# Performance work log

Measured on AMD Instinct MI355X. Metric: run time of the kernel, lower is better.

Reference implementation:

```python
import jax, jax.numpy as jnp
import numpy as np

NX, NY, NZ = 432, 496, 1   # grid_size (nx, ny, nz), nz must be 1
NBEV = 128                 # NUM_BEV_FEATURES
K = 4                      # NUM_K
SHRINK = 0.0025            # SHRINK_TH
BN_EPS = 1e-3


def setup_inputs():
    key = jax.random.key(0)
    ks = jax.random.split(key, 8)
    B, P, NPT, D, M = 2, 6000, 4096, 64, 1024
    pillar_features = jax.random.normal(ks[0], (B, P, D), jnp.float32)
    point_features = jax.random.normal(ks[1], (B, NPT, D), jnp.float32)
    # unique flat BEV cells per scene -> coords columns (z, y, x) as in OpenPCDet coords[:,1:4]
    coords = []
    for b in range(B):
        flat = jax.random.permutation(jax.random.fold_in(ks[2], b), NX * NY)[:P]
        y = flat // NX
        x = flat % NX
        z = jnp.zeros_like(flat)
        coords.append(jnp.stack([z, y, x], axis=1))
    voxel_coords = jnp.stack(coords, 0).astype(jnp.int32)
    adapt_w = jax.random.normal(ks[3], (NBEV // 2, D * K), jnp.float32) * 0.05  # Linear(no bias)
    mem_w = jax.random.normal(ks[4], (M, D), jnp.float32) * 0.05               # MemoryUnit slots
    bn_gamma = jnp.ones((NBEV // 2,), jnp.float32)
    bn_beta = jnp.zeros((NBEV // 2,), jnp.float32)
    return dict(pillar_features=pillar_features, point_features=point_features,
                voxel_coords=voxel_coords, adapt_w=adapt_w, mem_w=mem_w,
                bn_gamma=bn_gamma, bn_beta=bn_beta)


def _forward(pillar_features, point_features, voxel_coords, adapt_w, mem_w, bn_gamma, bn_beta):
    def per_batch(pillars, points, coords):
        # pillars [P,D], points [Np,D], coords [P,3] = (z, y, x)
        # get_score: softmax over points dim, top-k points per pillar
        score = jax.nn.softmax(pillars @ points.T, axis=1)            # [P,Np]
        _, idx = jax.lax.top_k(score, K)                              # [P,K] (indices detached)
        pts = points[idx]                                             # [P,K,D]
        # MemoryUnit (MemAE-style): softmax attention over memory, hard-shrink-relu, L1 renorm
        x = pts.reshape(-1, points.shape[1])                          # [P*K,D]
        att = jax.nn.softmax(x @ mem_w.T, axis=1)                     # [P*K,M]
        shr = jax.nn.relu(att - SHRINK) * att / (jnp.abs(att - SHRINK) + 1e-12)
        att = shr / (jnp.sum(jnp.abs(shr), axis=1, keepdims=True) + 1e-12)
        mem_out = (att @ mem_w).reshape(pillars.shape[0], -1)         # [P, K*D]
        # adapt_layer (Linear, no bias) -> BatchNorm1d (training stats over pillars) -> ReLU
        h = mem_out @ adapt_w.T                                       # [P, NBEV//2]
        mu = jnp.mean(h, axis=0)
        var = jnp.var(h, axis=0)
        h = (h - mu) / jnp.sqrt(var + BN_EPS) * bn_gamma + bn_beta
        h = jax.nn.relu(h)
        feats = jnp.concatenate([pillars, h], axis=1)                 # [P, NBEV]
        # scatter into dense BEV grid: index = z + y*nx + x (nz==1 so z==0)
        flat = coords[:, 0] + coords[:, 1] * NX + coords[:, 2]
        spatial = jnp.zeros((NBEV, NZ * NX * NY), feats.dtype).at[:, flat].set(feats.T)
        pind = jnp.zeros((3, NZ * NX * NY), feats.dtype)
        pind = pind.at[0, flat].set(coords[:, 1].astype(feats.dtype))
        pind = pind.at[1, flat].set(coords[:, 2].astype(feats.dtype))
        pind = pind.at[2, flat].set(coords[:, 0].astype(feats.dtype))
        return spatial, pind

    spatial, pind = jax.vmap(per_batch)(pillar_features, point_features, voxel_coords)
    B = spatial.shape[0]
    return spatial.reshape(B, NBEV * NZ, NY, NX), pind.reshape(B, 3 * NZ, NY, NX)


def reference(pillar_features, point_features, voxel_coords, adapt_w, mem_w, bn_gamma, bn_beta):
    return _forward(pillar_features, point_features, voxel_coords, adapt_w, mem_w, bn_gamma, bn_beta)
```

## Files before the change

kernel.cpp:

```cpp
#include <hip/hip_runtime.h>

#define NXg 432
#define NYg 496
#define SCELLS (NXg*NYg)
#define PB 6000
#define NPTS 4096
#define DD 64
#define MM 1024
#define KK 4
#define BB 2
#define NROWS (PB*KK)
#define NSEG 16
#define SEGPTS (NPTS/NSEG)
#define CHROWS 64
#define NCHNK (SEGPTS/CHROWS)
#define SHRINK_TH 0.0025f
#define BN_EPS 1e-3f
#define NEG_INF -3.402823466e38f

#define INS4(v, id, v0,v1,v2,v3, i0,i1,i2,i3) { \
    bool g0 = (v) > v0, g1 = (v) > v1, g2 = (v) > v2; \
    v3 = g2 ? v2 : (v);              i3 = g2 ? i2 : (id); \
    v2 = g2 ? (g1 ? v1 : (v)) : v2;  i2 = g2 ? (g1 ? i1 : (id)) : i2; \
    v1 = g1 ? (g0 ? v0 : (v)) : v1;  i1 = g1 ? (g0 ? i0 : (id)) : i1; \
    v0 = g0 ? (v) : v0;              i0 = g0 ? (id) : i0; \
}

__global__ __launch_bounds__(256) void k_init_inv(int* __restrict__ inv) {
    int i = blockIdx.x*256 + threadIdx.x;
    inv[i] = -1;
}

__global__ __launch_bounds__(256) void k_scatter_inv(const int* __restrict__ coords,
                                                     int* __restrict__ inv) {
    int i = blockIdx.x*256 + threadIdx.x;
    if (i >= BB*PB) return;
    int b = i / PB, p = i % PB;
    const int* c = coords + (size_t)i*3;
    int flat = c[0] + c[1]*NXg + c[2];
    inv[b*SCELLS + flat] = p;
}

__global__ __launch_bounds__(256) void k_score_topk(const float* __restrict__ pillars,
                                                    const float* __restrict__ points,
                                                    float* __restrict__ pV,
                                                    int* __restrict__ pI) {
    __shared__ float4 sPt[CHROWS*16];
    const int b = blockIdx.y;
    const int seg = blockIdx.z;
    const int t = threadIdx.x;
    const int pillar = blockIdx.x*256 + t;
    const int prow = pillar < PB ? pillar : PB-1;
    const int j0 = seg * SEGPTS;

    const float4* pil4  = (const float4*)pillars;
    const float4* ptsB4 = (const float4*)(points + (size_t)b*NPTS*DD);

    float4 wreg[16];
    #pragma unroll
    for (int d4 = 0; d4 < 16; d4++)
        wreg[d4] = pil4[((size_t)b*PB + prow)*16 + d4];

    float tv0=NEG_INF, tv1=NEG_INF, tv2=NEG_INF, tv3=NEG_INF;
    int   ti0=0, ti1=0, ti2=0, ti3=0;

    for (int ch = 0; ch < NCHNK; ch++) {
        const float4* src = ptsB4 + (size_t)(j0 + ch*CHROWS)*16;
        for (int i = t; i < CHROWS*16; i += 256)
            sPt[i] = src[i];
        __syncthreads();

        const int jb = j0 + ch*CHROWS;
        for (int j = 0; j < CHROWS; j += 2) {
            float a0 = 0.f, a1 = 0.f;
            #pragma unroll
            for (int d4 = 0; d4 < 16; d4++) {
                float4 x0 = sPt[j*16 + d4];
                float4 x1 = sPt[(j+1)*16 + d4];
                a0 += wreg[d4].x*x0.x + wreg[d4].y*x0.y + wreg[d4].z*x0.z + wreg[d4].w*x0.w;
                a1 += wreg[d4].x*x1.x + wreg[d4].y*x1.y + wreg[d4].z*x1.z + wreg[d4].w*x1.w;
            }
            if (a0 > tv3) INS4(a0, jb+j,   tv0,tv1,tv2,tv3, ti0,ti1,ti2,ti3)
            if (a1 > tv3) INS4(a1, jb+j+1, tv0,tv1,tv2,tv3, ti0,ti1,ti2,ti3)
        }
        __syncthreads();
    }

    if (pillar < PB) {
        size_t ob = (((size_t)b*NSEG + seg)*PB + pillar)*KK;
        pV[ob+0]=tv0; pV[ob+1]=tv1; pV[ob+2]=tv2; pV[ob+3]=tv3;
        pI[ob+0]=ti0; pI[ob+1]=ti1; pI[ob+2]=ti2; pI[ob+3]=ti3;
    }
}

__global__ __launch_bounds__(256) void k_merge(const float* __restrict__ pV,
                                               const int* __restrict__ pI,
                                               int* __restrict__ idxOut) {
    int i = blockIdx.x*256 + threadIdx.x;
    if (i >= BB*PB) return;
    int b = i / PB, p = i % PB;
    float fv0=NEG_INF, fv1=NEG_INF, fv2=NEG_INF, fv3=NEG_INF;
    int fi0=0, fi1=0, fi2=0, fi3=0;
    for (int s = 0; s < NSEG; s++) {
        size_t base = (((size_t)b*NSEG + s)*PB + p)*KK;
        #pragma unroll
        for (int q = 0; q < 4; q++) {
            float v = pV[base+q];
            if (v > fv3) INS4(v, pI[base+q], fv0,fv1,fv2,fv3, fi0,fi1,fi2,fi3)
        }
    }
    idxOut[(size_t)i*KK+0]=fi0; idxOut[(size_t)i*KK+1]=fi1;
    idxOut[(size_t)i*KK+2]=fi2; idxOut[(size_t)i*KK+3]=fi3;
}

__global__ __launch_bounds__(256) void k_logits(const float* __restrict__ points,
                                                const int* __restrict__ idxIn,
                                                const float* __restrict__ memw,
                                                float* __restrict__ logits,
                                                int b) {
    __shared__ float4 sX4[64*16];
    __shared__ int sId[64];
    const int t = threadIdx.x;
    const int lane = t & 63, wv = t >> 6;
    const int row0 = blockIdx.x * 64;
    const int cg = blockIdx.y * 256 + wv * 64;

    if (t < 64) sId[t] = idxIn[(size_t)b*NROWS + row0 + t];

    const float4* mw4 = (const float4*)memw;
    float4 wreg[16];
    #pragma unroll
    for (int d4 = 0; d4 < 16; d4++) wreg[d4] = mw4[(size_t)(cg + lane)*16 + d4];

    __syncthreads();
    const float4* ptsB4 = (const float4*)(points + (size_t)b*NPTS*DD);
    for (int i = t; i < 1024; i += 256) {
        int r = i >> 4, c = i & 15;
        sX4[i] = ptsB4[(size_t)sId[r]*16 + c];
    }
    __syncthreads();

    for (int r = 0; r < 64; r += 2) {
        float a0 = 0.f, a1 = 0.f;
        #pragma unroll
        for (int d4 = 0; d4 < 16; d4++) {
            float4 x0 = sX4[r*16 + d4];
            float4 x1 = sX4[(r+1)*16 + d4];
            a0 += wreg[d4].x*x0.x + wreg[d4].y*x0.y + wreg[d4].z*x0.z + wreg[d4].w*x0.w;
            a1 += wreg[d4].x*x1.x + wreg[d4].y*x1.y + wreg[d4].z*x1.z + wreg[d4].w*x1.w;
        }
        logits[(size_t)(row0 + r)*MM + cg + lane] = a0;
        logits[(size_t)(row0 + r + 1)*MM + cg + lane] = a1;
    }
}

__global__ __launch_bounds__(256) void k_mo(const float* __restrict__ logits,
                                            const float* __restrict__ memw,
                                            const float* __restrict__ adaptw,
                                            float* __restrict__ hOut,
                                            int b) {
    __shared__ __align__(16) char smem[77824];
    float4* sAtt4 = (float4*)smem;
    float4* sW4   = (float4*)(smem + 12288);
    float*  sWf   = (float*)sW4;
    __shared__ float sM[48], sRinv[48], sRsc[48];
    const int t = threadIdx.x;
    const int lane = t & 63, wv = t >> 6;
    const int p0 = blockIdx.x * 12;
    const int row0 = p0 * 4;

    const float4* lg4 = (const float4*)logits;
    #pragma unroll
    for (int rr = 0; rr < 12; rr++) {
        int r = wv*12 + rr;
        size_t base = (size_t)(row0 + r)*256;
        float4 l0 = lg4[base + lane];
        float4 l1 = lg4[base + 64 + lane];
        float4 l2 = lg4[base + 128 + lane];
        float4 l3 = lg4[base + 192 + lane];
        float m = fmaxf(fmaxf(fmaxf(l0.x,l0.y),fmaxf(l0.z,l0.w)),
                 fmaxf(fmaxf(fmaxf(l1.x,l1.y),fmaxf(l1.z,l1.w)),
                 fmaxf(fmaxf(fmaxf(l2.x,l2.y),fmaxf(l2.z,l2.w)),
                       fmaxf(fmaxf(l3.x,l3.y),fmaxf(l3.z,l3.w)))));
        #pragma unroll
        for (int off = 1; off < 64; off <<= 1) m = fmaxf(m, __shfl_xor(m, off));
        l0.x=__expf(l0.x-m); l0.y=__expf(l0.y-m); l0.z=__expf(l0.z-m); l0.w=__expf(l0.w-m);
        l1.x=__expf(l1.x-m); l1.y=__expf(l1.y-m); l1.z=__expf(l1.z-m); l1.w=__expf(l1.w-m);
        l2.x=__expf(l2.x-m); l2.y=__expf(l2.y-m); l2.z=__expf(l2.z-m); l2.w=__expf(l2.w-m);
        l3.x=__expf(l3.x-m); l3.y=__expf(l3.y-m); l3.z=__expf(l3.z-m); l3.w=__expf(l3.w-m);
        float s = (l0.x+l0.y+l0.z+l0.w) + (l1.x+l1.y+l1.z+l1.w)
                + (l2.x+l2.y+l2.z+l2.w) + (l3.x+l3.y+l3.z+l3.w);
        #pragma unroll
        for (int off = 1; off < 64; off <<= 1) s += __shfl_xor(s, off);
        float rinv = 1.f / s;
        float sh = 0.f;
        {
            float e, tt;
            e=l0.x*rinv; tt=e-SHRINK_TH; sh += tt>0.f ? e*tt/(tt+1e-12f) : 0.f;
            e=l0.y*rinv; tt=e-SHRINK_TH; sh += tt>0.f ? e*tt/(tt+1e-12f) : 0.f;
            e=l0.z*rinv; tt=e-SHRINK_TH; sh += tt>0.f ? e*tt/(tt+1e-12f) : 0.f;
            e=l0.w*rinv; tt=e-SHRINK_TH; sh += tt>0.f ? e*tt/(tt+1e-12f) : 0.f;
            e=l1.x*rinv; tt=e-SHRINK_TH; sh += tt>0.f ? e*tt/(tt+1e-12f) : 0.f;
            e=l1.y*rinv; tt=e-SHRINK_TH; sh += tt>0.f ? e*tt/(tt+1e-12f) : 0.f;
            e=l1.z*rinv; tt=e-SHRINK_TH; sh += tt>0.f ? e*tt/(tt+1e-12f) : 0.f;
            e=l1.w*rinv; tt=e-SHRINK_TH; sh += tt>0.f ? e*tt/(tt+1e-12f) : 0.f;
            e=l2.x*rinv; tt=e-SHRINK_TH; sh += tt>0.f ? e*tt/(tt+1e-12f) : 0.f;
            e=l2.y*rinv; tt=e-SHRINK_TH; sh += tt>0.f ? e*tt/(tt+1e-12f) : 0.f;
            e=l2.z*rinv; tt=e-SHRINK_TH; sh += tt>0.f ? e*tt/(tt+1e-12f) : 0.f;
            e=l2.w*rinv; tt=e-SHRINK_TH; sh += tt>0.f ? e*tt/(tt+1e-12f) : 0.f;
            e=l3.x*rinv; tt=e-SHRINK_TH; sh += tt>0.f ? e*tt/(tt+1e-12f) : 0.f;
            e=l3.y*rinv; tt=e-SHRINK_TH; sh += tt>0.f ? e*tt/(tt+1e-12f) : 0.f;
            e=l3.z*rinv; tt=e-SHRINK_TH; sh += tt>0.f ? e*tt/(tt+1e-12f) : 0.f;
            e=l3.w*rinv; tt=e-SHRINK_TH; sh += tt>0.f ? e*tt/(tt+1e-12f) : 0.f;
        }
        #pragma unroll
        for (int off = 1; off < 64; off <<= 1) sh += __shfl_xor(sh, off);
        if (lane == 0) { sM[r] = m; sRinv[r] = rinv; sRsc[r] = 1.f/(sh + 1e-12f); }
    }
    __syncthreads();

    float acc[12];
    #pragma unroll
    for (int s=0;s<12;s++) acc[s]=0.f;
    const float4* mw4 = (const float4*)memw;

    for (int tile = 0; tile < 16; tile++) {
        __syncthreads();
        for (int i = t; i < 768; i += 256) {
            int rr = i >> 4, m4 = i & 15;
            float4 lg = lg4[(size_t)(row0 + rr)*256 + tile*16 + m4];
            float m = sM[rr], rinv = sRinv[rr], rsc = sRsc[rr];
            float4 o;
            float e, tt;
            e=__expf(lg.x-m)*rinv; tt=e-SHRINK_TH; o.x = (tt>0.f ? e*tt/(tt+1e-12f) : 0.f)*rsc;
            e=__expf(lg.y-m)*rinv; tt=e-SHRINK_TH; o.y = (tt>0.f ? e*tt/(tt+1e-12f) : 0.f)*rsc;
            e=__expf(lg.z-m)*rinv; tt=e-SHRINK_TH; o.z = (tt>0.f ? e*tt/(tt+1e-12f) : 0.f)*rsc;
            e=__expf(lg.w-m)*rinv; tt=e-SHRINK_TH; o.w = (tt>0.f ? e*tt/(tt+1e-12f) : 0.f)*rsc;
            sAtt4[rr*16 + m4] = o;
        }
        #pragma unroll 4
        for (int i = t; i < 1024; i += 256) {
            int m = i >> 4, c4 = i & 15;
            sW4[m*16 + c4] = mw4[(size_t)(tile*64 + m)*16 + c4];
        }
        __syncthreads();
        #pragma unroll 4
        for (int m4 = 0; m4 < 16; m4++) {
            float w0 = sWf[(m4*4+0)*64 + lane];
            float w1 = sWf[(m4*4+1)*64 + lane];
            float w2 = sWf[(m4*4+2)*64 + lane];
            float w3 = sWf[(m4*4+3)*64 + lane];
            #pragma unroll
            for (int s = 0; s < 12; s++) {
                float4 a4 = sAtt4[(wv + 4*s)*16 + m4];
                acc[s] += a4.x*w0 + a4.y*w1 + a4.z*w2 + a4.w*w3;
            }
        }
    }
    __syncthreads();
    float* sMo = (float*)smem;
    float4* sA4 = (float4*)(smem + 12288);
    #pragma unroll
    for (int s = 0; s < 12; s++) {
        int r = wv + 4*s;
        sMo[r*64 + lane] = acc[s];
    }
    const float4* adG4 = (const float4*)adaptw;
    for (int i = t; i < 4096; i += 256) {
        int c = i >> 6, j4 = i & 63;
        sA4[c*64 + (j4 ^ (c & 15))] = adG4[c*64 + j4];
    }
    __syncthreads();
    const float4* sMo4 = (const float4*)sMo;
    float h0=0.f, h1=0.f, h2=0.f;
    #pragma unroll 8
    for (int j4 = 0; j4 < 64; j4++) {
        float4 a4 = sA4[lane*64 + (j4 ^ (lane & 15))];
        int sub = (j4 >> 4)*16 + (j4 & 15);
        float4 q0 = sMo4[(4*(wv+0))*16 + sub];
        float4 q1 = sMo4[(4*(wv+4))*16 + sub];
        float4 q2 = sMo4[(4*(wv+8))*16 + sub];
        h0 += q0.x*a4.x + q0.y*a4.y + q0.z*a4.z + q0.w*a4.w;
        h1 += q1.x*a4.x + q1.y*a4.y + q1.z*a4.z + q1.w*a4.w;
        h2 += q2.x*a4.x + q2.y*a4.y + q2.z*a4.z + q2.w*a4.w;
    }
    hOut[((size_t)b*PB + p0 + wv + 0)*DD + lane] = h0;
    hOut[((size_t)b*PB + p0 + wv + 4)*DD + lane] = h1;
    hOut[((size_t)b*PB + p0 + wv + 8)*DD + lane] = h2;
}

__global__ __launch_bounds__(256) void k_bn1(const float* __restrict__ h,
                                             float* __restrict__ pSum,
                                             float* __restrict__ pSq) {
    const int bid = blockIdx.x;
    const int b = bid >> 5, ch = bid & 31;
    const int r0 = ch*188;
    int r1 = r0 + 188; if (r1 > PB) r1 = PB;
    __shared__ float sS[4*64], sS2[4*64];
    const int t = threadIdx.x;
    const int c = t & 63, stripe = t >> 6;
    float s = 0.f, s2 = 0.f;
    for (int r = r0 + stripe; r < r1; r += 4) {
        float v = h[((size_t)b*PB + r)*DD + c];
        s += v; s2 += v*v;
    }
    sS[stripe*64 + c] = s; sS2[stripe*64 + c] = s2;
    __syncthreads();
    if (t < 64) {
        float ts = sS[t] + sS[64+t] + sS[128+t] + sS[192+t];
        float ts2 = sS2[t] + sS2[64+t] + sS2[128+t] + sS2[192+t];
        pSum[(size_t)bid*64 + t] = ts;
        pSq[(size_t)bid*64 + t] = ts2;
    }
}

__global__ __launch_bounds__(64) void k_bn2(const float* __restrict__ pSum,
                                            const float* __restrict__ pSq,
                                            const float* __restrict__ gamma,
                                            float* __restrict__ bnMu,
                                            float* __restrict__ bnScale) {
    const int b = blockIdx.x;
    const int t = threadIdx.x;
    float ts = 0.f, ts2 = 0.f;
    for (int ch = 0; ch < 32; ch++) {
        ts += pSum[(size_t)(b*32 + ch)*64 + t];
        ts2 += pSq[(size_t)(b*32 + ch)*64 + t];
    }
    float mu = ts / (float)PB;
    float var = ts2 / (float)PB - mu*mu;
    if (var < 0.f) var = 0.f;
    bnMu[b*64+t] = mu;
    bnScale[b*64+t] = gamma[t] / sqrtf(var + BN_EPS);
}

__global__ __launch_bounds__(256) void k_fill(const int* __restrict__ inv,
                                              const float* __restrict__ pillars,
                                              const float* __restrict__ h,
                                              const float* __restrict__ bnMu,
                                              const float* __restrict__ bnScale,
                                              const float* __restrict__ beta,
                                              float* __restrict__ out) {
    const int b = blockIdx.y;
    const int f = blockIdx.x*256 + threadIdx.x;
    __shared__ float sMu[64], sSc[64], sBe[64];
    if (threadIdx.x < 64) {
        sMu[threadIdx.x] = bnMu[b*64+threadIdx.x];
        sSc[threadIdx.x] = bnScale[b*64+threadIdx.x];
        sBe[threadIdx.x] = beta[threadIdx.x];
    }
    __syncthreads();
    int iv = inv[b*SCELLS + f];
    bool occ = iv >= 0;
    int iv0 = occ ? iv : 0;
    float* sp = out + (size_t)b*128*SCELLS;
    const float* prow = pillars + ((size_t)b*PB + iv0)*DD;
    const float* hrow = h + ((size_t)b*PB + iv0)*DD;
    #pragma unroll 4
    for (int c = 0; c < 64; c++)
        sp[(size_t)c*SCELLS + f] = occ ? prow[c] : 0.f;
    #pragma unroll 4
    for (int c = 0; c < 64; c++) {
        float v = 0.f;
        if (occ) {
            float hv = hrow[c];
            v = fmaxf((hv - sMu[c])*sSc[c] + sBe[c], 0.f);
        }
        sp[(size_t)(64+c)*SCELLS + f] = v;
    }
    float* pi = out + (size_t)BB*128*SCELLS + (size_t)b*3*SCELLS;
    pi[f]              = occ ? (float)(f / NXg) : 0.f;
    pi[SCELLS + f]     = occ ? (float)(f % NXg) : 0.f;
    pi[2*(size_t)SCELLS + f] = 0.f;
}

extern "C" void kernel_launch(void* const* d_in, const int* in_sizes, int n_in,
                              void* d_out, int out_size, void* d_ws, size_t ws_size,
                              hipStream_t stream) {
    const float* pillars = (const float*)d_in[0];
    const float* points  = (const float*)d_in[1];
    const int*   coords  = (const int*)d_in[2];
    const float* adaptw  = (const float*)d_in[3];
    const float* memw    = (const float*)d_in[4];
    const float* gamma   = (const float*)d_in[5];
    const float* beta    = (const float*)d_in[6];
    float* out = (float*)d_out;

    char* w = (char*)d_ws;
    int* inv = (int*)w;        w += (size_t)BB*SCELLS*4;
    int* idx = (int*)w;        w += (size_t)BB*PB*KK*4;
    float* h = (float*)w;      w += (size_t)BB*PB*DD*4;
    float* bnMu = (float*)w;   w += (size_t)BB*64*4;
    float* bnScale = (float*)w; w += (size_t)BB*64*4;
    float* pSum = (float*)w;   w += (size_t)BB*32*64*4;
    float* pSq = (float*)w;    w += (size_t)BB*32*64*4;
    float* logits = (float*)w;
    float* pV = logits;
    int*   pI = (int*)(logits + (size_t)BB*NSEG*PB*KK);

    k_init_inv<<<dim3(BB*SCELLS/256), dim3(256), 0, stream>>>(inv);
    k_scatter_inv<<<dim3((BB*PB+255)/256), dim3(256), 0, stream>>>(coords, inv);
    k_score_topk<<<dim3((PB+255)/256, BB, NSEG), dim3(256), 0, stream>>>(pillars, points, pV, pI);
    k_merge<<<dim3((BB*PB+255)/256), dim3(256), 0, stream>>>(pV, pI, idx);
    for (int b = 0; b < BB; b++) {
        k_logits<<<dim3(NROWS/64, 4), dim3(256), 0, stream>>>(points, idx, memw, logits, b);
        k_mo<<<dim3(PB/12), dim3(256), 0, stream>>>(logits, memw, adaptw, h, b);
    }
    k_bn1<<<dim3(BB*32), dim3(256), 0, stream>>>(h, pSum, pSq);
    k_bn2<<<dim3(BB), dim3(64), 0, stream>>>(pSum, pSq, gamma, bnMu, bnScale);
    k_fill<<<dim3(SCELLS/256, BB), dim3(256), 0, stream>>>(inv, pillars, h, bnMu, bnScale, beta, out);
}
```

Baseline: 761.1 us.

## Split memory-attention kernel into stats pass and smaller-tile attention kernel

Replaces the monolithic k_mo kernel, which used about 76 KB of shared memory for 48 rows per block, with a separate softmax-statistics kernel (one wave per row) and a k_att kernel handling 32 rows per block with a small shared footprint. The memory matrix is pre-transposed once so each lane holds its output channel's weights in registers per chunk instead of staging them in LDS, and adapt_w is read directly from global. The aim is higher occupancy and more blocks to hide latency, at the cost of an extra launch, rereading the logits, and more redundant global weight loads per block.

```diff
diff --git a/kernel.cpp b/kernel.cpp
--- a/kernel.cpp
+++ b/kernel.cpp
@@ -14,6 +14,9 @@
 #define SEGPTS (NPTS/NSEG)
 #define CHROWS 64
 #define NCHNK (SEGPTS/CHROWS)
+#define AROWS 32
+#define ACH 64
+#define NACH (MM/ACH)
 #define SHRINK_TH 0.0025f
 #define BN_EPS 1e-3f
 #define NEG_INF -3.402823466e38f
@@ -154,139 +157,148 @@
     }
 }
 
-__global__ __launch_bounds__(256) void k_mo(const float* __restrict__ logits,
-                                            const float* __restrict__ memw,
-                                            const float* __restrict__ adaptw,
-                                            float* __restrict__ hOut,
-                                            int b) {
-    __shared__ __align__(16) char smem[77824];
-    float4* sAtt4 = (float4*)smem;
-    float4* sW4   = (float4*)(smem + 12288);
-    float*  sWf   = (float*)sW4;
-    __shared__ float sM[48], sRinv[48], sRsc[48];
+__global__ __launch_bounds__(256) void k_transw(const float* __restrict__ memw,
+                                                float* __restrict__ memwT) {
+    int i = blockIdx.x*256 + threadIdx.x;
+    int d = i >> 10, m = i & 1023;
+    memwT[i] = memw[m*64 + d];
+}
+
+__global__ __launch_bounds__(256) void k_stats(const float* __restrict__ logits,
+                                               float* __restrict__ stats,
+                                               int b) {
+    const int wv = threadIdx.x >> 6, lane = threadIdx.x & 63;
+    const int row = blockIdx.x*4 + wv;
+    const float4* lg4 = (const float4*)logits;
+    size_t base = (size_t)row*256;
+    float4 l0 = lg4[base + lane];
+    float4 l1 = lg4[base + 64 + lane];
+    float4 l2 = lg4[base + 128 + lane];
+    float4 l3 = lg4[base + 192 + lane];
+    float m = fmaxf(fmaxf(fmaxf(l0.x,l0.y),fmaxf(l0.z,l0.w)),
+             fmaxf(fmaxf(fmaxf(l1.x,l1.y),fmaxf(l1.z,l1.w)),
+             fmaxf(fmaxf(fmaxf(l2.x,l2.y),fmaxf(l2.z,l2.w)),
+                   fmaxf(fmaxf(l3.x,l3.y),fmaxf(l3.z,l3.w)))));
+    #pragma unroll
+    for (int off = 1; off < 64; off <<= 1) m = fmaxf(m, __shfl_xor(m, off));
+    l0.x=__expf(l0.x-m); l0.y=__expf(l0.y-m); l0.z=__expf(l0.z-m); l0.w=__expf(l0.w-m);
+    l1.x=__expf(l1.x-m); l1.y=__expf(l1.y-m); l1.z=__expf(l1.z-m); l1.w=__expf(l1.w-m);
+    l2.x=__expf(l2.x-m); l2.y=__expf(l2.y-m); l2.z=__expf(l2.z-m); l2.w=__expf(l2.w-m);
+    l3.x=__expf(l3.x-m); l3.y=__expf(l3.y-m); l3.z=__expf(l3.z-m); l3.w=__expf(l3.w-m);
+    float s = (l0.x+l0.y+l0.z+l0.w) + (l1.x+l1.y+l1.z+l1.w)
+            + (l2.x+l2.y+l2.z+l2.w) + (l3.x+l3.y+l3.z+l3.w);
+    #pragma unroll
+    for (int off = 1; off < 64; off <<= 1) s += __shfl_xor(s, off);
+    float rinv = 1.f / s;
+    float sh = 0.f;
+    {
+        float e, tt;
+        e=l0.x*rinv; tt=e-SHRINK_TH; sh += tt>0.f ? e*tt/(tt+1e-12f) : 0.f;
+        e=l0.y*rinv; tt=e-SHRINK_TH; sh += tt>0.f ? e*tt/(tt+1e-12f) : 0.f;
+        e=l0.z*rinv; tt=e-SHRINK_TH; sh += tt>0.f ? e*tt/(tt+1e-12f) : 0.f;
+        e=l0.w*rinv; tt=e-SHRINK_TH; sh += tt>0.f ? e*tt/(tt+1e-12f) : 0.f;
+        e=l1.x*rinv; tt=e-SHRINK_TH; sh += tt>0.f ? e*tt/(tt+1e-12f) : 0.f;
+        e=l1.y*rinv; tt=e-SHRINK_TH; sh += tt>0.f ? e*tt/(tt+1e-12f) : 0.f;
+        e=l1.z*rinv; tt=e-SHRINK_TH; sh += tt>0.f ? e*tt/(tt+1e-12f) : 0.f;
+        e=l1.w*rinv; tt=e-SHRINK_TH; sh += tt>0.f ? e*tt/(tt+1e-12f) : 0.f;
+        e=l2.x*rinv; tt=e-SHRINK_TH; sh += tt>0.f ? e*tt/(tt+1e-12f) : 0.f;
+        e=l2.y*rinv; tt=e-SHRINK_TH; sh += tt>0.f ? e*tt/(tt+1e-12f) : 0.f;
+        e=l2.z*rinv; tt=e-SHRINK_TH; sh += tt>0.f ? e*tt/(tt+1e-12f) : 0.f;
+        e=l2.w*rinv; tt=e-SHRINK_TH; sh += tt>0.f ? e*tt/(tt+1e-12f) : 0.f;
+        e=l3.x*rinv; tt=e-SHRINK_TH; sh += tt>0.f ? e*tt/(tt+1e-12f) : 0.f;
+        e=l3.y*rinv; tt=e-SHRINK_TH; sh += tt>0.f ? e*tt/(tt+1e-12f) : 0.f;
+        e=l3.z*rinv; tt=e-SHRINK_TH; sh += tt>0.f ? e*tt/(tt+1e-12f) : 0.f;
+        e=l3.w*rinv; tt=e-SHRINK_TH; sh += tt>0.f ? e*tt/(tt+1e-12f) : 0.f;
+    }
+    #pragma unroll
+    for (int off = 1; off < 64; off <<= 1) sh += __shfl_xor(sh, off);
+    if (lane == 0) {
+        float4* st4 = (float4*)stats;
+        st4[(size_t)b*NROWS + row] = make_float4(m, rinv, 1.f/(sh + 1e-12f), 0.f);
+    }
+}
+
+__global__ __launch_bounds__(256) void k_att(const float* __restrict__ logits,
+                                             const float* __restrict__ memwT,
+                                             const float* __restrict__ stats,
+                                             const float* __restrict__ adaptw,
+                                             float* __restrict__ hOut,
+                                             int b) {
+    __shared__ float4 sAtt4[AROWS*16];
+    __shared__ float  sSt[AROWS*4];
     const int t = threadIdx.x;
     const int lane = t & 63, wv = t >> 6;
-    const int p0 = blockIdx.x * 12;
-    const int row0 = p0 * 4;
-
-    const float4* lg4 = (const float4*)logits;
-    #pragma unroll
-    for (int rr = 0; rr < 12; rr++) {
-        int r = wv*12 + rr;
-        size_t base = (size_t)(row0 + r)*256;
-        float4 l0 = lg4[base + lane];
-        float4 l1 = lg4[base + 64 + lane];
-        float4 l2 = lg4[base + 128 + lane];
-        float4 l3 = lg4[base + 192 + lane];
-        float m = fmaxf(fmaxf(fmaxf(l0.x,l0.y),fmaxf(l0.z,l0.w)),
-                 fmaxf(fmaxf(fmaxf(l1.x,l1.y),fmaxf(l1.z,l1.w)),
-                 fmaxf(fmaxf(fmaxf(l2.x,l2.y),fmaxf(l2.z,l2.w)),
-                       fmaxf(fmaxf(l3.x,l3.y),fmaxf(l3.z,l3.w)))));
+    const int rows0 = blockIdx.x * AROWS;
+    const int p0 = rows0 >> 2;
+
+    if (t < AROWS) {
+        const float4* st4 = (const float4*)stats;
+        float4 s = st4[(size_t)b*NROWS + rows0 + t];
+        sSt[t*4+0] = s.x; sSt[t*4+1] = s.y; sSt[t*4+2] = s.z; sSt[t*4+3] = s.w;
+    }
+
+    const float4* lg4  = (const float4*)logits;
+    const float4* mwT4 = (const float4*)memwT;
+
+    float acc[8];
+    #pragma unroll
+    for (int r = 0; r < 8; r++) acc[r] = 0.f;
+
+    __syncthreads();
+
+    for (int ch = 0; ch < NACH; ch++) {
+        const int m04 = ch * (ACH/4);
         #pragma unroll
-        for (int off = 1; off < 64; off <<= 1) m = fmaxf(m, __shfl_xor(m, off));
-        l0.x=__expf(l0.x-m); l0.y=__expf(l0.y-m); l0.z=__expf(l0.z-m); l0.w=__expf(l0.w-m);
-        l1.x=__expf(l1.x-m); l1.y=__expf(l1.y-m); l1.z=__expf(l1.z-m); l1.w=__expf(l1.w-m);
-        l2.x=__expf(l2.x-m); l2.y=__expf(l2.y-m); l2.z=__expf(l2.z-m); l2.w=__expf(l2.w-m);
-        l3.x=__expf(l3.x-m); l3.y=__expf(l3.y-m); l3.z=__expf(l3.z-m); l3.w=__expf(l3.w-m);
-        float s = (l0.x+l0.y+l0.z+l0.w) + (l1.x+l1.y+l1.z+l1.w)
-                + (l2.x+l2.y+l2.z+l2.w) + (l3.x+l3.y+l3.z+l3.w);
+        for (int q = 0; q < 2; q++) {
+            int idx = q*256 + t;
+            int row = idx >> 4, m4 = idx & 15;
+            float4 lg = lg4[(size_t)(rows0 + row)*256 + m04 + m4];
+            float m = sSt[row*4], rinv = sSt[row*4+1], rsc = sSt[row*4+2];
+            float4 o; float e, tt;
+            e=__expf(lg.x-m)*rinv; tt=e-SHRINK_TH; o.x=(tt>0.f?e*tt/(tt+1e-12f):0.f)*rsc;
+            e=__expf(lg.y-m)*rinv; tt=e-SHRINK_TH; o.y=(tt>0.f?e*tt/(tt+1e-12f):0.f)*rsc;
+            e=__expf(lg.z-m)*rinv; tt=e-SHRINK_TH; o.z=(tt>0.f?e*tt/(tt+1e-12f):0.f)*rsc;
+            e=__expf(lg.w-m)*rinv; tt=e-SHRINK_TH; o.w=(tt>0.f?e*tt/(tt+1e-12f):0.f)*rsc;
+            sAtt4[row*16 + m4] = o;
+        }
+        float4 wreg[16];
         #pragma unroll
-        for (int off = 1; off < 64; off <<= 1) s += __shfl_xor(s, off);
-        float rinv = 1.f / s;
-        float sh = 0.f;
-        {
-            float e, tt;
-            e=l0.x*rinv; tt=e-SHRINK_TH; sh += tt>0.f ? e*tt/(tt+1e-12f) : 0.f;
-            e=l0.y*rinv; tt=e-SHRINK_TH; sh += tt>0.f ? e*tt/(tt+1e-12f) : 0.f;
-            e=l0.z*rinv; tt=e-SHRINK_TH; sh += tt>0.f ? e*tt/(tt+1e-12f) : 0.f;
-            e=l0.w*rinv; tt=e-SHRINK_TH; sh += tt>0.f ? e*tt/(tt+1e-12f) : 0.f;
-            e=l1.x*rinv; tt=e-SHRINK_TH; sh += tt>0.f ? e*tt/(tt+1e-12f) : 0.f;
-            e=l1.y*rinv; tt=e-SHRINK_TH; sh += tt>0.f ? e*tt/(tt+1e-12f) : 0.f;
-            e=l1.z*rinv; tt=e-SHRINK_TH; sh += tt>0.f ? e*tt/(tt+1e-12f) : 0.f;
-            e=l1.w*rinv; tt=e-SHRINK_TH; sh += tt>0.f ? e*tt/(tt+1e-12f) : 0.f;
-            e=l2.x*rinv; tt=e-SHRINK_TH; sh += tt>0.f ? e*tt/(tt+1e-12f) : 0.f;
-            e=l2.y*rinv; tt=e-SHRINK_TH; sh += tt>0.f ? e*tt/(tt+1e-12f) : 0.f;
-            e=l2.z*rinv; tt=e-SHRINK_TH; sh += tt>0.f ? e*tt/(tt+1e-12f) : 0.f;
-            e=l2.w*rinv; tt=e-SHRINK_TH; sh += tt>0.f ? e*tt/(tt+1e-12f) : 0.f;
-            e=l3.x*rinv; tt=e-SHRINK_TH; sh += tt>0.f ? e*tt/(tt+1e-12f) : 0.f;
-            e=l3.y*rinv; tt=e-SHRINK_TH; sh += tt>0.f ? e*tt/(tt+1e-12f) : 0.f;
-            e=l3.z*rinv; tt=e-SHRINK_TH; sh += tt>0.f ? e*tt/(tt+1e-12f) : 0.f;
-            e=l3.w*rinv; tt=e-SHRINK_TH; sh += tt>0.f ? e*tt/(tt+1e-12f) : 0.f;
-        }
+        for (int i = 0; i < 16; i++)
+            wreg[i] = mwT4[(size_t)lane*256 + m04 + i];
+        __syncthreads();
         #pragma unroll
-        for (int off = 1; off < 64; off <<= 1) sh += __shfl_xor(sh, off);
-        if (lane == 0) { sM[r] = m; sRinv[r] = rinv; sRsc[r] = 1.f/(sh + 1e-12f); }
-    }
-    __syncthreads();
-
-    float acc[12];
-    #pragma unroll
-    for (int s=0;s<12;s++) acc[s]=0.f;
-    const float4* mw4 = (const float4*)memw;
-
-    for (int tile = 0; tile < 16; tile++) {
+        for (int r = 0; r < 8; r++) {
+            int row = wv*8 + r;
+            float a = 0.f;
+            #pragma unroll
+            for (int i = 0; i < 16; i++) {
+                float4 x = sAtt4[row*16 + i];
+                a += wreg[i].x*x.x + wreg[i].y*x.y + wreg[i].z*x.z + wreg[i].w*x.w;
+            }
+            acc[r] += a;
+        }
         __syncthreads();
-        for (int i = t; i < 768; i += 256) {
-            int rr = i >> 4, m4 = i & 15;
-            float4 lg = lg4[(size_t)(row0 + rr)*256 + tile*16 + m4];
-            float m = sM[rr], rinv = sRinv[rr], rsc = sRsc[rr];
-            float4 o;
-            float e, tt;
-            e=__expf(lg.x-m)*rinv; tt=e-SHRINK_TH; o.x = (tt>0.f ? e*tt/(tt+1e-12f) : 0.f)*rsc;
-            e=__expf(lg.y-m)*rinv; tt=e-SHRINK_TH; o.y = (tt>0.f ? e*tt/(tt+1e-12f) : 0.f)*rsc;
-            e=__expf(lg.z-m)*rinv; tt=e-SHRINK_TH; o.z = (tt>0.f ? e*tt/(tt+1e-12f) : 0.f)*rsc;
-            e=__expf(lg.w-m)*rinv; tt=e-SHRINK_TH; o.w = (tt>0.f ? e*tt/(tt+1e-12f) : 0.f)*rsc;
-            sAtt4[rr*16 + m4] = o;
-        }
-        #pragma unroll 4
-        for (int i = t; i < 1024; i += 256) {
-            int m = i >> 4, c4 = i & 15;
-            sW4[m*16 + c4] = mw4[(size_t)(tile*64 + m)*16 + c4];
-        }
-        __syncthreads();
-        #pragma unroll 4
-        for (int m4 = 0; m4 < 16; m4++) {
-            float w0 = sWf[(m4*4+0)*64 + lane];
-            float w1 = sWf[(m4*4+1)*64 + lane];
-            float w2 = sWf[(m4*4+2)*64 + lane];
-            float w3 = sWf[(m4*4+3)*64 + lane];
-            #pragma unroll
-            for (int s = 0; s < 12; s++) {
-                float4 a4 = sAtt4[(wv + 4*s)*16 + m4];
-                acc[s] += a4.x*w0 + a4.y*w1 + a4.z*w2 + a4.w*w3;
-            }
-        }
-    }
-    __syncthreads();
-    float* sMo = (float*)smem;
-    float4* sA4 = (float4*)(smem + 12288);
-    #pragma unroll
-    for (int s = 0; s < 12; s++) {
-        int r = wv + 4*s;
-        sMo[r*64 + lane] = acc[s];
-    }
+    }
+
+    float* sMo = (float*)sAtt4;
+    #pragma unroll
+    for (int r = 0; r < 8; r++)
+        sMo[(wv*8 + r)*64 + lane] = acc[r];
+    __syncthreads();
+    const float4* sMo4 = (const float4*)sMo;
     const float4* adG4 = (const float4*)adaptw;
-    for (int i = t; i < 4096; i += 256) {
-        int c = i >> 6, j4 = i & 63;
-        sA4[c*64 + (j4 ^ (c & 15))] = adG4[c*64 + j4];
-    }
-    __syncthreads();
-    const float4* sMo4 = (const float4*)sMo;
-    float h0=0.f, h1=0.f, h2=0.f;
-    #pragma unroll 8
-    for (int j4 = 0; j4 < 64; j4++) {
-        float4 a4 = sA4[lane*64 + (j4 ^ (lane & 15))];
-        int sub = (j4 >> 4)*16 + (j4 & 15);
-        float4 q0 = sMo4[(4*(wv+0))*16 + sub];
-        float4 q1 = sMo4[(4*(wv+4))*16 + sub];
-        float4 q2 = sMo4[(4*(wv+8))*16 + sub];
-        h0 += q0.x*a4.x + q0.y*a4.y + q0.z*a4.z + q0.w*a4.w;
-        h1 += q1.x*a4.x + q1.y*a4.y + q1.z*a4.z + q1.w*a4.w;
-        h2 += q2.x*a4.x + q2.y*a4.y + q2.z*a4.z + q2.w*a4.w;
+    float h0 = 0.f, h1 = 0.f;
+    #pragma unroll
+    for (int d4 = 0; d4 < 64; d4++) {
+        float4 aw = adG4[(size_t)lane*64 + d4];
+        int k = d4 >> 4, sub = d4 & 15;
+        float4 q0 = sMo4[(4*(wv+0)+k)*16 + sub];
+        float4 q1 = sMo4[(4*(wv+4)+k)*16 + sub];
+        h0 += q0.x*aw.x + q0.y*aw.y + q0.z*aw.z + q0.w*aw.w;
+        h1 += q1.x*aw.x + q1.y*aw.y + q1.z*aw.z + q1.w*aw.w;
     }
     hOut[((size_t)b*PB + p0 + wv + 0)*DD + lane] = h0;
     hOut[((size_t)b*PB + p0 + wv + 4)*DD + lane] = h1;
-    hOut[((size_t)b*PB + p0 + wv + 8)*DD + lane] = h2;
 }
 
 __global__ __launch_bounds__(256) void k_bn1(const float* __restrict__ h,
@@ -393,6 +405,8 @@
     float* bnScale = (float*)w; w += (size_t)BB*64*4;
     float* pSum = (float*)w;   w += (size_t)BB*32*64*4;
     float* pSq = (float*)w;    w += (size_t)BB*32*64*4;
+    float* stats = (float*)w;  w += (size_t)BB*NROWS*4*4;
+    float* memwT = (float*)w;  w += (size_t)MM*DD*4;
     float* logits = (float*)w;
     float* pV = logits;
     int*   pI = (int*)(logits + (size_t)BB*NSEG*PB*KK);
@@ -401,9 +415,11 @@
     k_scatter_inv<<<dim3((BB*PB+255)/256), dim3(256), 0, stream>>>(coords, inv);
     k_score_topk<<<dim3((PB+255)/256, BB, NSEG), dim3(256), 0, stream>>>(pillars, points, pV, pI);
     k_merge<<<dim3((BB*PB+255)/256), dim3(256), 0, stream>>>(pV, pI, idx);
+    k_transw<<<dim3(MM*DD/256), dim3(256), 0, stream>>>(memw, memwT);
     for (int b = 0; b < BB; b++) {
         k_logits<<<dim3(NROWS/64, 4), dim3(256), 0, stream>>>(points, idx, memw, logits, b);
-        k_mo<<<dim3(PB/12), dim3(256), 0, stream>>>(logits, memw, adaptw, h, b);
+        k_stats<<<dim3(NROWS/4), dim3(256), 0, stream>>>(logits, stats, b);
+        k_att<<<dim3(NROWS/AROWS), dim3(256), 0, stream>>>(logits, memwT, stats, adaptw, h, b);
     }
     k_bn1<<<dim3(BB*32), dim3(256), 0, stream>>>(h, pSum, pSq);
     k_bn2<<<dim3(BB), dim3(64), 0, stream>>>(pSum, pSq, gamma, bnMu, bnScale);
```

Measured after the change: 831.1 us. 9.2% more time.
